# Performance work log

Hardware: AMD Instinct MI355X
Metric: run time of the kernel (lower is better)

## Reference

```python
import jax, jax.numpy as jnp
import numpy as np

NUM_HEADS = 12


def setup_inputs() -> dict:
    key = jax.random.key(0)
    ks = jax.random.split(key, 7)
    B, H, W, C = 1, 64, 64, 768
    hd = C // NUM_HEADS
    return {
        "x": jax.random.normal(ks[0], (B, H, W, C), dtype=jnp.float32),
        "qkv_w": jax.random.normal(ks[1], (C, 3 * C), dtype=jnp.float32) * 0.02,
        "qkv_b": jax.random.normal(ks[2], (3 * C,), dtype=jnp.float32) * 0.02,
        "proj_w": jax.random.normal(ks[3], (C, C), dtype=jnp.float32) * 0.02,
        "proj_b": jax.random.normal(ks[4], (C,), dtype=jnp.float32) * 0.02,
        "rel_pos_h": jax.random.normal(ks[5], (2 * H - 1, hd), dtype=jnp.float32) * 0.02,
        "rel_pos_w": jax.random.normal(ks[6], (2 * W - 1, hd), dtype=jnp.float32) * 0.02,
    }


def _rel_table(size, rel_pos):
    # q_size == k_size so relative_coords = i - j + (size - 1)
    coords = jnp.arange(size)[:, None] - jnp.arange(size)[None, :] + (size - 1)
    return rel_pos[coords]  # [size, size, head_dim]


def reference(x, qkv_w, qkv_b, proj_w, proj_b, rel_pos_h, rel_pos_w):
    B, H, W, C = x.shape
    nh = NUM_HEADS
    hd = C // nh
    scale = hd ** -0.5
    N = H * W

    qkv = x.reshape(B, N, C) @ qkv_w + qkv_b  # [B, N, 3C]
    qkv = qkv.reshape(B, N, 3, nh, hd).transpose(2, 0, 3, 1, 4).reshape(3, B * nh, N, hd)
    q, k, v = qkv[0], qkv[1], qkv[2]

    attn = jnp.einsum("bqd,bkd->bqk", q * scale, k)  # [B*nh, N, N]

    # decomposed relative position bias
    Rh = _rel_table(H, rel_pos_h)  # [H, H, hd]
    Rw = _rel_table(W, rel_pos_w)  # [W, W, hd]
    qr = q.reshape(B * nh, H, W, hd)
    rel_h = jnp.einsum("bhwc,hkc->bhwk", qr, Rh)  # [B*nh, H, W, H]
    rel_w = jnp.einsum("bhwc,wkc->bhwk", qr, Rw)  # [B*nh, H, W, W]
    bias = rel_h[..., :, None] + rel_w[..., None, :]  # [B*nh, H, W, H, W]
    attn = attn + bias.reshape(B * nh, N, N)

    attn = jax.nn.softmax(attn, axis=-1)
    out = jnp.einsum("bqk,bkd->bqd", attn, v)  # [B*nh, N, hd]
    out = out.reshape(B, nh, H, W, hd).transpose(0, 2, 3, 1, 4).reshape(B, H, W, C)
    return out @ proj_w + proj_b
```

## Files before the change

### kernel.cpp

```cpp
#include <hip/hip_runtime.h>
#include <math.h>

#define NHEADS 12
#define NTOK 4096
#define LOG2E 1.44269504f

typedef __attribute__((ext_vector_type(8))) short bf8v;
typedef __attribute__((ext_vector_type(4))) float f4v;
typedef __attribute__((ext_vector_type(16))) float f16v;

__device__ __forceinline__ unsigned short f2bf(float f) {
  unsigned int u = __float_as_uint(f);
  u += 0x7fffu + ((u >> 16) & 1u);
  return (unsigned short)(u >> 16);
}
__device__ __forceinline__ bf8v pack8(float4 a, float4 b) {
  bf8v v;
  v[0] = (short)f2bf(a.x); v[1] = (short)f2bf(a.y);
  v[2] = (short)f2bf(a.z); v[3] = (short)f2bf(a.w);
  v[4] = (short)f2bf(b.x); v[5] = (short)f2bf(b.y);
  v[6] = (short)f2bf(b.z); v[7] = (short)f2bf(b.w);
  return v;
}
__device__ __forceinline__ unsigned pkbf(float hi, float lo) {
  return __builtin_amdgcn_perm(__float_as_uint(hi) + 0x8000u,
                               __float_as_uint(lo) + 0x8000u, 0x07060302u);
}
__device__ __forceinline__ void gload_lds16(const void* g, void* l) {
  __builtin_amdgcn_global_load_lds(
      (const __attribute__((address_space(1))) void*)g,
      (__attribute__((address_space(3))) void*)l, 16, 0, 0);
}

__device__ __forceinline__ void tcvt_body(
    const float* __restrict__ in, short* __restrict__ out, int R, int C,
    int bx, int by, int t, float (*Ts)[65])
{
    const int bc = bx * 64, br = by * 64;
    {
        const int r = t >> 2, c0 = (t & 3) * 16;
        const float* src = in + (size_t)(br + r) * C + bc + c0;
#pragma unroll
        for (int i = 0; i < 4; ++i) {
            float4 a = *(const float4*)(src + 4 * i);
            Ts[r][c0 + 4 * i + 0] = a.x;
            Ts[r][c0 + 4 * i + 1] = a.y;
            Ts[r][c0 + 4 * i + 2] = a.z;
            Ts[r][c0 + 4 * i + 3] = a.w;
        }
    }
    __syncthreads();
    const int c = t >> 2, r0 = (t & 3) * 16;
    short* dst = out + (size_t)(bc + c) * R + br + r0;
#pragma unroll
    for (int p = 0; p < 2; ++p) {
        bf8v v;
#pragma unroll
        for (int i = 0; i < 8; ++i) v[i] = (short)f2bf(Ts[r0 + p * 8 + i][c]);
        *(bf8v*)(dst + p * 8) = v;
    }
}

__global__ __launch_bounds__(256) void prep_kernel(
    const float* __restrict__ x, const float* __restrict__ qkvw,
    const float* __restrict__ pw, short* __restrict__ xh,
    short* __restrict__ wqkvT, short* __restrict__ pwT)
{
    __shared__ float Ts[64][65];
    const int bid = blockIdx.x, t = threadIdx.x;
    if (bid < 1536) {
        const size_t i = ((size_t)bid * 256 + t) * 8;
        float4 a = *(const float4*)(x + i);
        float4 b = *(const float4*)(x + i + 4);
        *(bf8v*)(xh + i) = pack8(a, b);
    } else if (bid < 1968) {
        const int idx = bid - 1536;
        tcvt_body(qkvw, wqkvT, 768, 2304, idx % 36, idx / 36, t, Ts);
    } else {
        const int idx = bid - 1968;
        tcvt_body(pw, pwT, 768, 768, idx % 12, idx / 12, t, Ts);
    }
}

__global__ __launch_bounds__(256) void qkv_mfma_kernel(
    const short* __restrict__ xh, const short* __restrict__ wT,
    const float* __restrict__ bias, short* __restrict__ qbh,
    short* __restrict__ kbh, short* __restrict__ vblk)
{
    __shared__ __align__(16) short As[128 * 32];
    __shared__ __align__(16) short Bs[96 * 32];
    const int t = threadIdx.x;
    const int w = t >> 6, lane = t & 63;
    const int l15 = lane & 15, l4 = lane >> 4;
    const int wr = w >> 1, wc = w & 1;
    const int row0 = blockIdx.y * 128, col0 = blockIdx.x * 96;
    const int ldr = lane >> 2;
    const int ldk = (lane & 3) * 8;

    f4v acc[4][3] = {};
    const short* aBase = xh + (size_t)(row0 + w * 32 + ldr) * 768 + ldk;
    const short* bBase0 = wT + (size_t)(col0 + w * 16 + ldr) * 768 + ldk;
    const short* bBase1 = wT + (size_t)(col0 + 64 + w * 16 + ldr) * 768 + ldk;

    for (int kk = 0; kk < 768; kk += 32) {
        __syncthreads();
#pragma unroll
        for (int c = 0; c < 2; ++c)
            gload_lds16(aBase + (size_t)c * 16 * 768 + kk,
                        &As[(w * 32 + c * 16) * 32]);
        gload_lds16(bBase0 + kk, &Bs[(w * 16) * 32]);
        if (w < 2)
            gload_lds16(bBase1 + kk, &Bs[(64 + w * 16) * 32]);
        __syncthreads();
        bf8v af[4], bg[3];
#pragma unroll
        for (int i = 0; i < 4; ++i)
            af[i] = *(const bf8v*)&As[(wr * 64 + 16 * i + l15) * 32 + l4 * 8];
#pragma unroll
        for (int j = 0; j < 3; ++j)
            bg[j] = *(const bf8v*)&Bs[(wc * 48 + 16 * j + l15) * 32 + l4 * 8];
#pragma unroll
        for (int i = 0; i < 4; ++i)
#pragma unroll
            for (int j = 0; j < 3; ++j)
                acc[i][j] = __builtin_amdgcn_mfma_f32_16x16x32_bf16(
                    af[i], bg[j], acc[i][j], 0, 0, 0);
    }

#pragma unroll
    for (int j = 0; j < 3; ++j) {
        const int n = col0 + wc * 48 + 16 * j + l15;
        const int s = n / 768;
        const int rm = n - s * 768;
        const int h = rm >> 6, d = rm & 63;
        const float bv = bias[n];
        if (s == 2) {
#pragma unroll
            for (int i = 0; i < 4; ++i) {
                const int m = row0 + wr * 64 + 16 * i + l4 * 4;
                short4 pv;
                pv.x = (short)f2bf(acc[i][j][0] + bv);
                pv.y = (short)f2bf(acc[i][j][1] + bv);
                pv.z = (short)f2bf(acc[i][j][2] + bv);
                pv.w = (short)f2bf(acc[i][j][3] + bv);
                *(short4*)(vblk +
                           ((size_t)(h * 256 + (m >> 4)) * 64 + d) * 16 +
                           (m & 15)) = pv;
            }
        } else {
            short* dst = (s == 0) ? qbh : kbh;
#pragma unroll
            for (int i = 0; i < 4; ++i) {
                const int m = row0 + wr * 64 + 16 * i + l4 * 4;
#pragma unroll
                for (int r = 0; r < 4; ++r)
                    dst[((size_t)h * NTOK + m + r) * 64 + d] =
                        (short)f2bf(acc[i][j][r] + bv);
            }
        }
    }
}

union FlashSMem {
    struct {
        short Ks[128][68];
        float relHs[64][65];
    };
    float U[128 * 65];
    struct {
        float OEp[64][64];
        float lEp[64];
    };
};

__global__ __launch_bounds__(256, 3) void flash_mfma_kernel(
    const short* __restrict__ qbh, const short* __restrict__ kbh,
    const short* __restrict__ vblk, const float* __restrict__ rpw,
    const float* __restrict__ rph, short* __restrict__ aob)
{
    __shared__ __align__(16) FlashSMem sm;

    const int t = threadIdx.x;
    const int qt = blockIdx.x, head = blockIdx.y;
    const int row0 = qt * 64;
    const int lane = t & 63, w = t >> 6;
    const int qh2 = w & 1, th = w >> 1;
    const int l31 = lane & 31, hf = lane >> 5;
    const size_t hB = (size_t)head * NTOK * 64;
    const float SC = 0.125f * LOG2E;

    const int q = row0 + qh2 * 32 + l31;
    bf8v bQ[4];
    {
        const short* qsrc = qbh + hB + (size_t)q * 64;
#pragma unroll
        for (int ks = 0; ks < 4; ++ks)
            bQ[ks] = *(const bf8v*)(qsrc + ks * 16 + hf * 8);
    }
    const int sx = t >> 2;
    const int sck = (t & 3) * 16;
    const short* kptr = kbh + hB + (size_t)sx * 64 + sck;
    const short* vb2 = vblk + ((size_t)head * 256 * 64 + l31) * 16 + hf * 8;
    bf8v kpf[4];
    kpf[0] = *(const bf8v*)(kptr);
    kpf[1] = *(const bf8v*)(kptr + 8);
    kpf[2] = *(const bf8v*)(kptr + 64 * 64);
    kpf[3] = *(const bf8v*)(kptr + 64 * 64 + 8);

#pragma unroll
    for (int jt2 = 0; jt2 < 2; ++jt2) {
        const int jt = 2 * th + jt2;
        int j = jt * 32 + l31;
        if (j > 126) j = 0;
        const float* asrc = rpw + (size_t)j * 64;
        f16v c = {};
#pragma unroll
        for (int ks = 0; ks < 4; ++ks) {
            float4 u0 = *(const float4*)(asrc + ks * 16 + hf * 8);
            float4 u1 = *(const float4*)(asrc + ks * 16 + hf * 8 + 4);
            c = __builtin_amdgcn_mfma_f32_32x32x16_bf16(
                pack8(u0, u1), bQ[ks], c, 0, 0, 0);
        }
#pragma unroll
        for (int reg = 0; reg < 16; ++reg)
            sm.U[(jt * 32 + (reg & 3) + 8 * (reg >> 2) + 4 * hf) * 65 +
                 qh2 * 32 + l31] = c[reg];
    }
    __syncthreads();
    const int qw = qh2 * 32 + l31;
    uint2 rwp[2][4];
#pragma unroll
    for (int t32 = 0; t32 < 2; ++t32)
#pragma unroll
        for (int g = 0; g < 4; ++g) {
            const int kw = t32 * 32 + 8 * g + 4 * hf;
            const float v0 = sm.U[(qw + 63 - kw) * 65 + qw] * LOG2E;
            const float v1 = sm.U[(qw + 62 - kw) * 65 + qw] * LOG2E;
            const float v2 = sm.U[(qw + 61 - kw) * 65 + qw] * LOG2E;
            const float v3 = sm.U[(qw + 60 - kw) * 65 + qw] * LOG2E;
            rwp[t32][g].x = pkbf(v1, v0);
            rwp[t32][g].y = pkbf(v3, v2);
        }
    __syncthreads();

    {
        const int kh = th * 32 + l31;
        const float* asrc = rph + (size_t)(qt + 63 - kh) * 64;
        f16v c = {};
#pragma unroll
        for (int ks = 0; ks < 4; ++ks) {
            float4 u0 = *(const float4*)(asrc + ks * 16 + hf * 8);
            float4 u1 = *(const float4*)(asrc + ks * 16 + hf * 8 + 4);
            u0.x *= LOG2E; u0.y *= LOG2E; u0.z *= LOG2E; u0.w *= LOG2E;
            u1.x *= LOG2E; u1.y *= LOG2E; u1.z *= LOG2E; u1.w *= LOG2E;
            c = __builtin_amdgcn_mfma_f32_32x32x16_bf16(
                pack8(u0, u1), bQ[ks], c, 0, 0, 0);
        }
#pragma unroll
        for (int reg = 0; reg < 16; ++reg)
            sm.relHs[th * 32 + (reg & 3) + 8 * (reg >> 2) + 4 * hf]
                    [qh2 * 32 + l31] = c[reg];
    }

    f16v O[2] = {{}, {}};
    float lsum = 0.f;

    for (int it = 0; it < 32; ++it) {
        __syncthreads();
        *(bf8v*)&sm.Ks[sx][sck] = kpf[0];
        *(bf8v*)&sm.Ks[sx][sck + 8] = kpf[1];
        *(bf8v*)&sm.Ks[sx + 64][sck] = kpf[2];
        *(bf8v*)&sm.Ks[sx + 64][sck + 8] = kpf[3];
        {
            const int itn = (it < 31) ? it + 1 : 31;
            const short* kp = kptr + (size_t)itn * 128 * 64;
            kpf[0] = *(const bf8v*)kp;
            kpf[1] = *(const bf8v*)(kp + 8);
            kpf[2] = *(const bf8v*)(kp + 64 * 64);
            kpf[3] = *(const bf8v*)(kp + 64 * 64 + 8);
        }
        __syncthreads();

        f16v acc[2] = {{}, {}};
#pragma unroll
        for (int ks = 0; ks < 4; ++ks)
#pragma unroll
            for (int t32 = 0; t32 < 2; ++t32)
                acc[t32] = __builtin_amdgcn_mfma_f32_32x32x16_bf16(
                    *(const bf8v*)&sm.Ks[th * 64 + t32 * 32 + l31]
                                        [ks * 16 + hf * 8],
                    bQ[ks], acc[t32], 0, 0, 0);

        bf8v vB[2][2][2];
        {
            const short* vit = vb2 + (size_t)(it * 8 + th * 4) * 64 * 16;
#pragma unroll
            for (int t32 = 0; t32 < 2; ++t32)
#pragma unroll
                for (int ks2 = 0; ks2 < 2; ++ks2)
#pragma unroll
                    for (int nt = 0; nt < 2; ++nt)
                        vB[t32][ks2][nt] = *(const bf8v*)(
                            vit + ((size_t)(t32 * 2 + ks2) * 64 + nt * 32) *
                                      16);
        }

        const float rh = sm.relHs[2 * it + th][qh2 * 32 + l31];

        unsigned xg[2][4], yg[2][4];
#pragma unroll
        for (int t32 = 0; t32 < 2; ++t32) {
            float sub = 0.f;
#pragma unroll
            for (int g = 0; g < 4; ++g) {
                const unsigned u0 = rwp[t32][g].x;
                const unsigned u1 = rwp[t32][g].y;
                const float b0 = __uint_as_float(u0 << 16) + rh;
                const float b1 = __uint_as_float(u0 & 0xffff0000u) + rh;
                const float b2 = __uint_as_float(u1 << 16) + rh;
                const float b3 = __uint_as_float(u1 & 0xffff0000u) + rh;
                const float e0 = __builtin_amdgcn_exp2f(
                    fmaf(acc[t32][4 * g + 0], SC, b0));
                const float e1 = __builtin_amdgcn_exp2f(
                    fmaf(acc[t32][4 * g + 1], SC, b1));
                const float e2 = __builtin_amdgcn_exp2f(
                    fmaf(acc[t32][4 * g + 2], SC, b2));
                const float e3 = __builtin_amdgcn_exp2f(
                    fmaf(acc[t32][4 * g + 3], SC, b3));
                sub += (e0 + e1) + (e2 + e3);
                xg[t32][g] = pkbf(e1, e0);
                yg[t32][g] = pkbf(e3, e2);
            }
            lsum += sub;
        }

#pragma unroll
        for (int t32 = 0; t32 < 2; ++t32)
#pragma unroll
            for (int ks2 = 0; ks2 < 2; ++ks2) {
                auto px = __builtin_amdgcn_permlane32_swap(
                    xg[t32][2 * ks2], xg[t32][2 * ks2 + 1], false, false);
                auto py = __builtin_amdgcn_permlane32_swap(
                    yg[t32][2 * ks2], yg[t32][2 * ks2 + 1], false, false);
                int4 av;
                av.x = (int)px[0];
                av.y = (int)py[0];
                av.z = (int)px[1];
                av.w = (int)py[1];
                union { int4 i; bf8v v; } u; u.i = av;
#pragma unroll
                for (int nt = 0; nt < 2; ++nt)
                    O[nt] = __builtin_amdgcn_mfma_f32_32x32x16_bf16(
                        u.v, vB[t32][ks2][nt], O[nt], 0, 0, 0);
            }
    }

    lsum += __shfl_xor(lsum, 32);
    __syncthreads();
    if (th == 1) {
#pragma unroll
        for (int nt = 0; nt < 2; ++nt)
#pragma unroll
            for (int reg = 0; reg < 16; ++reg) {
                const int qr = (reg & 3) + 8 * (reg >> 2) + 4 * hf;
                sm.OEp[qh2 * 32 + qr][nt * 32 + l31] = O[nt][reg];
            }
        if (lane < 32) sm.lEp[qh2 * 32 + l31] = lsum;
    }
    __syncthreads();
    if (th == 0) {
        lsum += sm.lEp[qh2 * 32 + l31];
        const float linv = 1.0f / lsum;
#pragma unroll
        for (int nt = 0; nt < 2; ++nt)
#pragma unroll
            for (int reg = 0; reg < 16; ++reg) {
                const int qr = (reg & 3) + 8 * (reg >> 2) + 4 * hf;
                const float li = __shfl(linv, qr);
                const float o =
                    O[nt][reg] + sm.OEp[qh2 * 32 + qr][nt * 32 + l31];
                aob[(size_t)(row0 + qh2 * 32 + qr) * 768 + head * 64 +
                    nt * 32 + l31] = (short)f2bf(o * li);
            }
    }
}

__global__ __launch_bounds__(256) void proj_mfma_kernel(
    const short* __restrict__ aoh, const short* __restrict__ pwT,
    const float* __restrict__ bias, float* __restrict__ out)
{
    __shared__ __align__(16) short As[64 * 32];
    __shared__ __align__(16) short Bs[128 * 32];
    const int t = threadIdx.x;
    const int w = t >> 6, lane = t & 63;
    const int l15 = lane & 15, l4 = lane >> 4;
    const int wr = w >> 1, wc = w & 1;
    const int row0 = blockIdx.y * 64, col0 = blockIdx.x * 128;
    const int ldr = lane >> 2;
    const int ldk = (lane & 3) * 8;

    f4v acc[2][4] = {};
    const short* aBase = aoh + (size_t)(row0 + w * 16 + ldr) * 768 + ldk;
    const short* bBase = pwT + (size_t)(col0 + w * 32 + ldr) * 768 + ldk;

    for (int kk = 0; kk < 768; kk += 32) {
        __syncthreads();
        gload_lds16(aBase + kk, &As[(w * 16) * 32]);
#pragma unroll
        for (int c = 0; c < 2; ++c)
            gload_lds16(bBase + (size_t)c * 16 * 768 + kk,
                        &Bs[(w * 32 + c * 16) * 32]);
        __syncthreads();
        bf8v af[2], bg[4];
#pragma unroll
        for (int i = 0; i < 2; ++i)
            af[i] = *(const bf8v*)&As[(wr * 32 + 16 * i + l15) * 32 + l4 * 8];
#pragma unroll
        for (int j = 0; j < 4; ++j)
            bg[j] = *(const bf8v*)&Bs[(wc * 64 + 16 * j + l15) * 32 + l4 * 8];
#pragma unroll
        for (int i = 0; i < 2; ++i)
#pragma unroll
            for (int j = 0; j < 4; ++j)
                acc[i][j] = __builtin_amdgcn_mfma_f32_16x16x32_bf16(
                    af[i], bg[j], acc[i][j], 0, 0, 0);
    }

#pragma unroll
    for (int j = 0; j < 4; ++j) {
        const int n = col0 + wc * 64 + 16 * j + l15;
        const float bv = bias[n];
#pragma unroll
        for (int i = 0; i < 2; ++i) {
            const int m = row0 + wr * 32 + 16 * i + l4 * 4;
#pragma unroll
            for (int r = 0; r < 4; ++r)
                out[(size_t)(m + r) * 768 + n] = acc[i][j][r] + bv;
        }
    }
}

extern "C" void kernel_launch(void* const* d_in, const int* in_sizes, int n_in,
                              void* d_out, int out_size, void* d_ws,
                              size_t ws_size, hipStream_t stream)
{
    (void)in_sizes; (void)n_in; (void)out_size; (void)ws_size;
    const float* x    = (const float*)d_in[0];
    const float* qkvw = (const float*)d_in[1];
    const float* qkvb = (const float*)d_in[2];
    const float* pw   = (const float*)d_in[3];
    const float* pb   = (const float*)d_in[4];
    const float* rph  = (const float*)d_in[5];
    const float* rpw  = (const float*)d_in[6];
    float* out = (float*)d_out;

    const size_t S = (size_t)NHEADS * NTOK * 64;
    short* qbh  = (short*)d_ws;
    short* kbh  = qbh + S;
    short* vblk = kbh + S;
    short* xh   = vblk + S;
    short* aob  = xh;
    short* wqkvT = xh + S;
    short* pwT  = wqkvT + (size_t)2304 * 768;

    prep_kernel<<<dim3(2112), 256, 0, stream>>>(x, qkvw, pw, xh, wqkvT, pwT);
    qkv_mfma_kernel<<<dim3(24, 32), 256, 0, stream>>>(xh, wqkvT, qkvb,
                                                      qbh, kbh, vblk);
    flash_mfma_kernel<<<dim3(64, NHEADS), 256, 0, stream>>>(qbh, kbh, vblk,
                                                            rpw, rph, aob);
    proj_mfma_kernel<<<dim3(6, 64), 256, 0, stream>>>(aob, pwT, pb, out);
}
```

Baseline: 216.2 us.

## Store K in MFMA-fragment blocked layout and load it directly into registers

The QKV kernel now writes K in a blocked layout that matches the MFMA A-operand fragment. The flash kernel loads K fragments straight from global memory into registers with a one-iteration prefetch, which drops the LDS staging buffer and the two barriers per iteration. It also keeps the rel-pos W bias as fp32 in registers rather than packed bf16, and uses the hardware v_cvt_pk_bf16_f32 for packing the probabilities. The cost is higher register pressure (32 extra VGPRs for the bias, 2x K fragments) at 3 waves/SIMD, plus redundant global K loads across waves that were previously shared through LDS.

```diff
diff --git a/kernel.cpp b/kernel.cpp
--- a/kernel.cpp
+++ b/kernel.cpp
@@ -22,9 +22,10 @@
   v[6] = (short)f2bf(b.z); v[7] = (short)f2bf(b.w);
   return v;
 }
-__device__ __forceinline__ unsigned pkbf(float hi, float lo) {
-  return __builtin_amdgcn_perm(__float_as_uint(hi) + 0x8000u,
-                               __float_as_uint(lo) + 0x8000u, 0x07060302u);
+__device__ __forceinline__ unsigned cvtpk(float lo, float hi) {
+  unsigned r;
+  asm("v_cvt_pk_bf16_f32 %0, %1, %2" : "=v"(r) : "v"(lo), "v"(hi));
+  return r;
 }
 __device__ __forceinline__ void gload_lds16(const void* g, void* l) {
   __builtin_amdgcn_global_load_lds(
@@ -85,7 +86,7 @@
 __global__ __launch_bounds__(256) void qkv_mfma_kernel(
     const short* __restrict__ xh, const short* __restrict__ wT,
     const float* __restrict__ bias, short* __restrict__ qbh,
-    short* __restrict__ kbh, short* __restrict__ vblk)
+    short* __restrict__ kblk, short* __restrict__ vblk)
 {
     __shared__ __align__(16) short As[128 * 32];
     __shared__ __align__(16) short Bs[96 * 32];
@@ -147,25 +148,32 @@
                            ((size_t)(h * 256 + (m >> 4)) * 64 + d) * 16 +
                            (m & 15)) = pv;
             }
-        } else {
-            short* dst = (s == 0) ? qbh : kbh;
+        } else if (s == 0) {
 #pragma unroll
             for (int i = 0; i < 4; ++i) {
                 const int m = row0 + wr * 64 + 16 * i + l4 * 4;
 #pragma unroll
                 for (int r = 0; r < 4; ++r)
-                    dst[((size_t)h * NTOK + m + r) * 64 + d] =
+                    qbh[((size_t)h * NTOK + m + r) * 64 + d] =
                         (short)f2bf(acc[i][j][r] + bv);
             }
+        } else {
+#pragma unroll
+            for (int i = 0; i < 4; ++i) {
+                const int m = row0 + wr * 64 + 16 * i + l4 * 4;
+                short* dst = kblk +
+                    ((((size_t)(h * 128 + (m >> 5)) * 8 + (d >> 3)) * 32 +
+                      (m & 31)) * 8 + (d & 7));
+#pragma unroll
+                for (int r = 0; r < 4; ++r)
+                    dst[r * 8] = (short)f2bf(acc[i][j][r] + bv);
+            }
         }
     }
 }
 
 union FlashSMem {
-    struct {
-        short Ks[128][68];
-        float relHs[64][65];
-    };
+    float relHs[64][65];
     float U[128 * 65];
     struct {
         float OEp[64][64];
@@ -174,7 +182,7 @@
 };
 
 __global__ __launch_bounds__(256, 3) void flash_mfma_kernel(
-    const short* __restrict__ qbh, const short* __restrict__ kbh,
+    const short* __restrict__ qbh, const short* __restrict__ kblk,
     const short* __restrict__ vblk, const float* __restrict__ rpw,
     const float* __restrict__ rph, short* __restrict__ aob)
 {
@@ -197,15 +205,17 @@
         for (int ks = 0; ks < 4; ++ks)
             bQ[ks] = *(const bf8v*)(qsrc + ks * 16 + hf * 8);
     }
-    const int sx = t >> 2;
-    const int sck = (t & 3) * 16;
-    const short* kptr = kbh + hB + (size_t)sx * 64 + sck;
+
+    const short* kb = kblk + (size_t)head * 262144 + th * 4096 + hf * 256 +
+                      (size_t)l31 * 8;
+    bf8v kf[2][4];
+#pragma unroll
+    for (int t32 = 0; t32 < 2; ++t32)
+#pragma unroll
+        for (int ks = 0; ks < 4; ++ks)
+            kf[t32][ks] = *(const bf8v*)(kb + t32 * 2048 + ks * 512);
+
     const short* vb2 = vblk + ((size_t)head * 256 * 64 + l31) * 16 + hf * 8;
-    bf8v kpf[4];
-    kpf[0] = *(const bf8v*)(kptr);
-    kpf[1] = *(const bf8v*)(kptr + 8);
-    kpf[2] = *(const bf8v*)(kptr + 64 * 64);
-    kpf[3] = *(const bf8v*)(kptr + 64 * 64 + 8);
 
 #pragma unroll
     for (int jt2 = 0; jt2 < 2; ++jt2) {
@@ -228,18 +238,16 @@
     }
     __syncthreads();
     const int qw = qh2 * 32 + l31;
-    uint2 rwp[2][4];
+    float rwf[2][4][4];
 #pragma unroll
     for (int t32 = 0; t32 < 2; ++t32)
 #pragma unroll
         for (int g = 0; g < 4; ++g) {
             const int kw = t32 * 32 + 8 * g + 4 * hf;
-            const float v0 = sm.U[(qw + 63 - kw) * 65 + qw] * LOG2E;
-            const float v1 = sm.U[(qw + 62 - kw) * 65 + qw] * LOG2E;
-            const float v2 = sm.U[(qw + 61 - kw) * 65 + qw] * LOG2E;
-            const float v3 = sm.U[(qw + 60 - kw) * 65 + qw] * LOG2E;
-            rwp[t32][g].x = pkbf(v1, v0);
-            rwp[t32][g].y = pkbf(v3, v2);
+#pragma unroll
+            for (int e = 0; e < 4; ++e)
+                rwf[t32][g][e] =
+                    sm.U[(qw + 63 - kw - e) * 65 + qw] * LOG2E;
         }
     __syncthreads();
 
@@ -261,35 +269,30 @@
             sm.relHs[th * 32 + (reg & 3) + 8 * (reg >> 2) + 4 * hf]
                     [qh2 * 32 + l31] = c[reg];
     }
+    __syncthreads();
 
     f16v O[2] = {{}, {}};
     float lsum = 0.f;
 
     for (int it = 0; it < 32; ++it) {
-        __syncthreads();
-        *(bf8v*)&sm.Ks[sx][sck] = kpf[0];
-        *(bf8v*)&sm.Ks[sx][sck + 8] = kpf[1];
-        *(bf8v*)&sm.Ks[sx + 64][sck] = kpf[2];
-        *(bf8v*)&sm.Ks[sx + 64][sck + 8] = kpf[3];
+        f16v acc[2] = {{}, {}};
+#pragma unroll
+        for (int ks = 0; ks < 4; ++ks)
+#pragma unroll
+            for (int t32 = 0; t32 < 2; ++t32)
+                acc[t32] = __builtin_amdgcn_mfma_f32_32x32x16_bf16(
+                    kf[t32][ks], bQ[ks], acc[t32], 0, 0, 0);
+
         {
             const int itn = (it < 31) ? it + 1 : 31;
-            const short* kp = kptr + (size_t)itn * 128 * 64;
-            kpf[0] = *(const bf8v*)kp;
-            kpf[1] = *(const bf8v*)(kp + 8);
-            kpf[2] = *(const bf8v*)(kp + 64 * 64);
-            kpf[3] = *(const bf8v*)(kp + 64 * 64 + 8);
-        }
-        __syncthreads();
-
-        f16v acc[2] = {{}, {}};
-#pragma unroll
-        for (int ks = 0; ks < 4; ++ks)
+            const short* kp = kb + (size_t)itn * 8192;
 #pragma unroll
             for (int t32 = 0; t32 < 2; ++t32)
-                acc[t32] = __builtin_amdgcn_mfma_f32_32x32x16_bf16(
-                    *(const bf8v*)&sm.Ks[th * 64 + t32 * 32 + l31]
-                                        [ks * 16 + hf * 8],
-                    bQ[ks], acc[t32], 0, 0, 0);
+#pragma unroll
+                for (int ks = 0; ks < 4; ++ks)
+                    kf[t32][ks] =
+                        *(const bf8v*)(kp + t32 * 2048 + ks * 512);
+        }
 
         bf8v vB[2][2][2];
         {
@@ -305,7 +308,7 @@
                                       16);
         }
 
-        const float rh = sm.relHs[2 * it + th][qh2 * 32 + l31];
+        const float rh = sm.relHs[2 * it + th][qw];
 
         unsigned xg[2][4], yg[2][4];
 #pragma unroll
@@ -313,23 +316,17 @@
             float sub = 0.f;
 #pragma unroll
             for (int g = 0; g < 4; ++g) {
-                const unsigned u0 = rwp[t32][g].x;
-                const unsigned u1 = rwp[t32][g].y;
-                const float b0 = __uint_as_float(u0 << 16) + rh;
-                const float b1 = __uint_as_float(u0 & 0xffff0000u) + rh;
-                const float b2 = __uint_as_float(u1 << 16) + rh;
-                const float b3 = __uint_as_float(u1 & 0xffff0000u) + rh;
                 const float e0 = __builtin_amdgcn_exp2f(
-                    fmaf(acc[t32][4 * g + 0], SC, b0));
+                    fmaf(acc[t32][4 * g + 0], SC, rwf[t32][g][0] + rh));
                 const float e1 = __builtin_amdgcn_exp2f(
-                    fmaf(acc[t32][4 * g + 1], SC, b1));
+                    fmaf(acc[t32][4 * g + 1], SC, rwf[t32][g][1] + rh));
                 const float e2 = __builtin_amdgcn_exp2f(
-                    fmaf(acc[t32][4 * g + 2], SC, b2));
+                    fmaf(acc[t32][4 * g + 2], SC, rwf[t32][g][2] + rh));
                 const float e3 = __builtin_amdgcn_exp2f(
-                    fmaf(acc[t32][4 * g + 3], SC, b3));
+                    fmaf(acc[t32][4 * g + 3], SC, rwf[t32][g][3] + rh));
                 sub += (e0 + e1) + (e2 + e3);
-                xg[t32][g] = pkbf(e1, e0);
-                yg[t32][g] = pkbf(e3, e2);
+                xg[t32][g] = cvtpk(e0, e1);
+                yg[t32][g] = cvtpk(e2, e3);
             }
             lsum += sub;
         }
@@ -456,8 +453,8 @@
 
     const size_t S = (size_t)NHEADS * NTOK * 64;
     short* qbh  = (short*)d_ws;
-    short* kbh  = qbh + S;
-    short* vblk = kbh + S;
+    short* kblk = qbh + S;
+    short* vblk = kblk + S;
     short* xh   = vblk + S;
     short* aob  = xh;
     short* wqkvT = xh + S;
@@ -465,8 +462,8 @@
 
     prep_kernel<<<dim3(2112), 256, 0, stream>>>(x, qkvw, pw, xh, wqkvT, pwT);
     qkv_mfma_kernel<<<dim3(24, 32), 256, 0, stream>>>(xh, wqkvT, qkvb,
-                                                      qbh, kbh, vblk);
-    flash_mfma_kernel<<<dim3(64, NHEADS), 256, 0, stream>>>(qbh, kbh, vblk,
+                                                      qbh, kblk, vblk);
+    flash_mfma_kernel<<<dim3(64, NHEADS), 256, 0, stream>>>(qbh, kblk, vblk,
                                                             rpw, rph, aob);
     proj_mfma_kernel<<<dim3(6, 64), 256, 0, stream>>>(aob, pwT, pb, out);
 }
```

Result: no change. 217.9 us (+0.8%).
